# Kernel tuning notes

Measured on AMD Instinct MI355X. Metric: run time of the kernel, lower is better.

## Reference

```python
import jax, jax.numpy as jnp
import numpy as np
import math

D_MODEL, N_HEADS, D_HEAD = 768, 12, 64
INIT_RANGE = 0.02
ROPE_BASE = 10000.0


def _rope_cos_sin(seq_len, d_head, dtype=jnp.float32):
    # theta_j = base^(-2j/d), positions m -> angles [T, d/2]
    inv_freq = 1.0 / (ROPE_BASE ** (jnp.arange(0, d_head, 2, dtype=jnp.float32) / d_head))
    ang = jnp.arange(seq_len, dtype=jnp.float32)[:, None] * inv_freq[None, :]
    return jnp.cos(ang).astype(dtype), jnp.sin(ang).astype(dtype)


def _apply_rope(x, cos, sin):
    # x: [b, t, h, d]; rotate consecutive (even, odd) pairs as complex numbers
    xr, xi = x[..., 0::2], x[..., 1::2]
    c = cos[None, :, None, :]
    s = sin[None, :, None, :]
    out_r = xr * c - xi * s
    out_i = xr * s + xi * c
    return jnp.stack([out_r, out_i], axis=-1).reshape(x.shape)


def setup_inputs() -> dict:
    key = jax.random.key(0)
    ks = jax.random.split(key, 5)
    B, T = 2, 2048
    x = jax.random.normal(ks[0], (B, T, D_MODEL), dtype=jnp.float32)
    W_Q = INIT_RANGE * jax.random.normal(ks[1], (N_HEADS, D_MODEL, D_HEAD), dtype=jnp.float32)
    W_K = INIT_RANGE * jax.random.normal(ks[2], (N_HEADS, D_MODEL, D_HEAD), dtype=jnp.float32)
    W_V = INIT_RANGE * jax.random.normal(ks[3], (N_HEADS, D_MODEL, D_HEAD), dtype=jnp.float32)
    W_O = INIT_RANGE * jax.random.normal(ks[4], (N_HEADS, D_HEAD, D_MODEL), dtype=jnp.float32)
    b_Q = jnp.zeros((N_HEADS, D_HEAD), dtype=jnp.float32)
    b_K = jnp.zeros((N_HEADS, D_HEAD), dtype=jnp.float32)
    b_V = jnp.zeros((N_HEADS, D_HEAD), dtype=jnp.float32)
    b_O = jnp.zeros((D_MODEL,), dtype=jnp.float32)
    return {"normalized_resid_pre": x, "W_Q": W_Q, "b_Q": b_Q, "W_K": W_K, "b_K": b_K,
            "W_V": W_V, "b_V": b_V, "W_O": W_O, "b_O": b_O}


def reference(normalized_resid_pre, W_Q, b_Q, W_K, b_K, W_V, b_V, W_O, b_O):
    x = normalized_resid_pre
    B, T, _ = x.shape
    cos, sin = _rope_cos_sin(T, D_HEAD, x.dtype)
    Q = jnp.einsum('btc,hcd->bthd', x, W_Q) + b_Q
    K = jnp.einsum('btc,hcd->bthd', x, W_K) + b_K
    V = jnp.einsum('btc,hcd->bthd', x, W_V) + b_V
    Q = _apply_rope(Q, cos, sin)
    K = _apply_rope(K, cos, sin)
    scores = jnp.einsum('bqhd,bkhd->bhqk', Q, K) / math.sqrt(D_HEAD)
    # Faithful to source: tril zeros upper triangle, then all exact zeros -> -inf
    tril = jnp.tril(jnp.ones((T, T), dtype=bool))
    z = jnp.where(tril[None, None], scores, 0.0)
    z = jnp.where(z == 0.0, -jnp.inf, z)
    probs = jax.nn.softmax(z, axis=-1)
    o = jnp.einsum('bhqk,bkhd->bqhd', probs, V)
    return jnp.einsum('bqhd,hdm->bqm', o, W_O) + b_O
```

## Files before the change

### kernel.cpp

```cpp
#include <hip/hip_runtime.h>

typedef unsigned short u16;
typedef unsigned int u32;
typedef short bf16x8 __attribute__((ext_vector_type(8)));
typedef float f32x4 __attribute__((ext_vector_type(4)));
typedef float f32x16 __attribute__((ext_vector_type(16)));

#define MFMA(a, b, c) __builtin_amdgcn_mfma_f32_16x16x32_bf16(a, b, c, 0, 0, 0)
#define MFMA32(a, b, c) __builtin_amdgcn_mfma_f32_32x32x16_bf16(a, b, c, 0, 0, 0)

__device__ __forceinline__ u16 f2bf(float f) {
  unsigned int u = __float_as_uint(f);
  u = (u + 0x7FFFu + ((u >> 16) & 1u)) >> 16;
  return (u16)u;
}

#define GLOAD16(gp, lp)                                                        \
  __builtin_amdgcn_global_load_lds(                                            \
      (const __attribute__((address_space(1))) void*)(gp),                     \
      (__attribute__((address_space(3))) void*)(lp), 16, 0, 0)


__global__ void rope_tables(float* __restrict__ cost, float* __restrict__ sint) {
  int idx = blockIdx.x * 256 + threadIdx.x;
  if (idx >= 2048 * 32) return;
  int t = idx >> 5, i = idx & 31;
  float invf = expf(-(float)i * 0.28782313662425572f);
  float ang = (float)t * invf;
  cost[idx] = cosf(ang);
  sint[idx] = sinf(ang);
}

__global__ void cast_x(const float* __restrict__ x, u16* __restrict__ xb, int n) {
  int i = (blockIdx.x * 256 + threadIdx.x) * 4;
  if (i >= n) return;
  float4 v = *(const float4*)(x + i);
  u16 o0 = f2bf(v.x), o1 = f2bf(v.y), o2 = f2bf(v.z), o3 = f2bf(v.w);
  ushort4 o = make_ushort4(o0, o1, o2, o3);
  *(ushort4*)(xb + i) = o;
}

__global__ void prep_wqkv(const float* __restrict__ WQ, const float* __restrict__ WK,
                          const float* __restrict__ WV, u16* __restrict__ Wt) {
  __shared__ float tile[32][33];
  const int z = blockIdx.z;
  const int qkv = z / 12, h = z - qkv * 12;
  const float* W = (qkv == 0 ? WQ : qkv == 1 ? WK : WV) + (size_t)h * 768 * 64;
  const int k0 = blockIdx.x * 32, d0 = blockIdx.y * 32;
  const int tx = threadIdx.x, ty = threadIdx.y;
#pragma unroll
  for (int it = 0; it < 4; it++)
    tile[ty + it * 8][tx] = W[(size_t)(k0 + ty + it * 8) * 64 + d0 + tx];
  __syncthreads();
  u16* out = Wt + (size_t)(qkv * 768 + h * 64 + d0) * 768 + k0;
#pragma unroll
  for (int it = 0; it < 4; it++)
    out[(size_t)(ty + it * 8) * 768 + tx] = f2bf(tile[tx][ty + it * 8]);
}

__global__ void prep_wo(const float* __restrict__ WO, u16* __restrict__ Wt) {
  __shared__ float tile[32][33];
  const int a0 = blockIdx.x * 32, m0 = blockIdx.y * 32;
  const int tx = threadIdx.x, ty = threadIdx.y;
#pragma unroll
  for (int it = 0; it < 4; it++)
    tile[ty + it * 8][tx] = WO[(size_t)(a0 + ty + it * 8) * 768 + m0 + tx];
  __syncthreads();
#pragma unroll
  for (int it = 0; it < 4; it++)
    Wt[(size_t)(m0 + ty + it * 8) * 768 + a0 + tx] = f2bf(tile[tx][ty + it * 8]);
}

template <int MODE>
__global__ __launch_bounds__(256) void gemm_bt(
    const u16* __restrict__ A, const u16* __restrict__ Bt, int K, int LDA, int LDB,
    const float* __restrict__ bQ, const float* __restrict__ bK, const float* __restrict__ bV,
    const float* __restrict__ cost, const float* __restrict__ sint,
    u16* __restrict__ Qb, u16* __restrict__ Kb, u16* __restrict__ Vt,
    const float* __restrict__ bO, float* __restrict__ Out) {
  __shared__ u16 As[128 * 32];
  __shared__ u16 Bs[128 * 32];
  const int tid = threadIdx.x;
  const int w = tid >> 6, l = tid & 63;
  const int lr = l >> 4, lc = l & 15;
  const int wr = w >> 1, wc = w & 1;
  const int m0 = blockIdx.x * 128, n0 = blockIdx.y * 128;

  f32x4 acc[4][4];
#pragma unroll
  for (int mi = 0; mi < 4; mi++)
#pragma unroll
    for (int ni = 0; ni < 4; ni++) acc[mi][ni] = (f32x4){0.f, 0.f, 0.f, 0.f};

  for (int kt = 0; kt < K; kt += 32) {
    const u16* ga = A + (size_t)(m0 + w * 16 + (l >> 2)) * LDA + kt + (l & 3) * 8;
    const u16* gb = Bt + (size_t)(n0 + w * 16 + (l >> 2)) * LDB + kt + (l & 3) * 8;
    GLOAD16(ga, &As[w * 512]);
    GLOAD16(ga + (size_t)64 * LDA, &As[2048 + w * 512]);
    GLOAD16(gb, &Bs[w * 512]);
    GLOAD16(gb + (size_t)64 * LDB, &Bs[2048 + w * 512]);
    __syncthreads();

    bf16x8 af[4], bfr[4];
#pragma unroll
    for (int mi = 0; mi < 4; mi++)
      af[mi] = *(const bf16x8*)&As[(wr * 64 + mi * 16 + lc) * 32 + lr * 8];
#pragma unroll
    for (int ni = 0; ni < 4; ni++)
      bfr[ni] = *(const bf16x8*)&Bs[(wc * 64 + ni * 16 + lc) * 32 + lr * 8];
#pragma unroll
    for (int mi = 0; mi < 4; mi++)
#pragma unroll
      for (int ni = 0; ni < 4; ni++)
        acc[mi][ni] = MFMA(af[mi], bfr[ni], acc[mi][ni]);
    __syncthreads();
  }

#pragma unroll
  for (int mi = 0; mi < 4; mi++) {
#pragma unroll
    for (int ni = 0; ni < 4; ni++) {
      const int col = n0 + wc * 64 + ni * 16 + lc;
      const int rowb = m0 + wr * 64 + mi * 16 + lr * 4;
      if (MODE == 0) {
        const int qkv = col / 768;
        const int rem = col - qkv * 768;
        const int h = rem >> 6, d = rem & 63, fi = d >> 1;
        const float bb = (qkv == 0 ? bQ : qkv == 1 ? bK : bV)[rem];
#pragma unroll
        for (int r = 0; r < 4; r++) {
          const int grow = rowb + r;
          const int t = grow & 2047;
          float v = acc[mi][ni][r] + bb;
          float pv = __shfl_xor(v, 1);
          if (qkv < 2) {
            const float c = cost[t * 32 + fi], s = sint[t * 32 + fi];
            float o = (d & 1) ? (pv * s + v * c) : (v * c - pv * s);
            if (qkv == 0) o *= 0.125f;
            (qkv == 0 ? Qb : Kb)[(size_t)grow * 768 + rem] = f2bf(o);
          } else {
            const int bidx = grow >> 11;
            Vt[((size_t)(bidx * 12 + h) * 64 + d) * 2048 + t] = f2bf(v);
          }
        }
      } else {
        const float bb = bO[col];
#pragma unroll
        for (int r = 0; r < 4; r++) {
          const int grow = rowb + r;
          Out[(size_t)grow * 768 + col] = acc[mi][ni][r] + bb;
        }
      }
    }
  }
}

__global__ __launch_bounds__(256, 2) void attn_kernel(
    const u16* __restrict__ Qb, const u16* __restrict__ Kb,
    const u16* __restrict__ Vt, u16* __restrict__ Ob) {
  __shared__ char Kls[4][8192];
  __shared__ char Vls[4][8192];
  char* scratch = (char*)Kls;

  const int id = blockIdx.x + 16 * blockIdx.y;
  const int s_ = id >> 3;
  const int bh = (id & 7) + 8 * (s_ % 3);
  const int xq = s_ / 3;
  const int b = bh / 12, h = bh - b * 12;
  const int tid = threadIdx.x, w = tid >> 6, l = tid & 63;
  const int lq = l & 31, hi = l >> 5;
  const int qhalf = w & 1, grp = w >> 1;

  const u16* kbase = Kb + (size_t)(b * 2048) * 768 + h * 64;
  const u16* vbase = Vt + (size_t)(bh * 64) * 2048;

  const int r8 = l >> 3;
  const int scol8 = (l & 7) ^ r8;
  const u16* ksrc = kbase + (size_t)(w * 16 + r8) * 768 + scol8 * 8;
  const u16* vsrc = vbase + (size_t)(w * 16 + r8) * 2048 + scol8 * 8;

#define STAGE(t, bi)                                                        \
  {                                                                         \
    const size_t ko = (size_t)(t) * 64 * 768;                               \
    const int vo = (t) * 64;                                                \
    GLOAD16(ksrc + ko,            &Kls[bi][w * 2048]);                      \
    GLOAD16(ksrc + ko + 8 * 768,  &Kls[bi][w * 2048 + 1024]);               \
    GLOAD16(vsrc + vo,            &Vls[bi][w * 2048]);                      \
    GLOAD16(vsrc + vo + 8 * 2048, &Vls[bi][w * 2048 + 1024]);               \
  }

  const int fswz = (lq & 7) << 4;

#pragma unroll 1
  for (int half = 0; half < 2; half++) {
    const int qblk = half == 0 ? 31 - xq : xq;
    const int n = qblk + 1;
    const int nsup = (n + 1) >> 1;

    bf16x8 qf[4];
    {
      const u16* qp = Qb + ((size_t)(b * 2048 + qblk * 64 + qhalf * 32 + lq)) * 768 +
                      h * 64 + hi * 8;
#pragma unroll
      for (int c = 0; c < 4; c++) qf[c] = *(const bf16x8*)(qp + c * 16);
    }

    float m_run = -INFINITY, l_run = 0.f;
    f32x16 acc2[2];
    acc2[0] = (f32x16)0.0f;
    acc2[1] = (f32x16)0.0f;

    STAGE(0, 0);
    if (n > 1) STAGE(1, 1);

    for (int p = 0; p < nsup; p++) {
      const int t0 = 2 * p;
      asm volatile("s_waitcnt vmcnt(0)" ::: "memory");
      __builtin_amdgcn_s_barrier();
      __builtin_amdgcn_sched_barrier(0);
      if (t0 + 2 < n) STAGE(t0 + 2, (t0 + 2) & 3);
      if (t0 + 3 < n) STAGE(t0 + 3, (t0 + 3) & 3);

      const int tile = t0 + grp;
      if (tile < n) {
        const int cur = tile & 3;

        f32x16 s2[2];
        s2[0] = (f32x16)0.0f;
        s2[1] = (f32x16)0.0f;
        __builtin_amdgcn_s_setprio(1);
#pragma unroll
        for (int c = 0; c < 4; c++) {
          const int cb = (c * 32 + hi * 16) ^ fswz;
          bf16x8 kf0 = *(const bf16x8*)(&Kls[cur][lq * 128] + cb);
          bf16x8 kf1 = *(const bf16x8*)(&Kls[cur][(32 + lq) * 128] + cb);
          s2[0] = MFMA32(kf0, qf[c], s2[0]);
          s2[1] = MFMA32(kf1, qf[c], s2[1]);
        }
        __builtin_amdgcn_s_setprio(0);

        if (tile == qblk) {
          const int qrel = qhalf * 32 + lq;
#pragma unroll
          for (int kt2 = 0; kt2 < 2; kt2++)
#pragma unroll
            for (int r = 0; r < 16; r++) {
              const int ko = kt2 * 32 + (r & 3) + 8 * (r >> 2) + 4 * hi;
              if (ko > qrel) s2[kt2][r] = -INFINITY;
            }
        }

        float pm = s2[0][0];
#pragma unroll
        for (int r = 1; r < 16; r++) pm = fmaxf(pm, s2[0][r]);
#pragma unroll
        for (int r = 0; r < 16; r++) pm = fmaxf(pm, s2[1][r]);
        pm = fmaxf(pm, __shfl_xor(pm, 32));

        const float mn = fmaxf(m_run, pm);
        const float alpha = __expf(m_run - mn);
        m_run = mn;

        float rs = 0.f;
        u32 pk[2][8];
#pragma unroll
        for (int kt2 = 0; kt2 < 2; kt2++)
#pragma unroll
          for (int j = 0; j < 8; j++) {
            float p0 = __expf(s2[kt2][2 * j] - mn);
            float p1 = __expf(s2[kt2][2 * j + 1] - mn);
            rs += p0 + p1;
            asm("v_cvt_pk_bf16_f32 %0, %1, %2" : "=v"(pk[kt2][j]) : "v"(p0), "v"(p1));
          }
        l_run = l_run * alpha + rs;

        union { u32 u[4]; bf16x8 v; } pf[4];
#pragma unroll
        for (int kq = 0; kq < 4; kq++) {
          const int kt2 = kq >> 1, i0 = 4 * (kq & 1);
          u32 a0 = pk[kt2][i0], b0 = pk[kt2][i0 + 2];
          u32 a1 = pk[kt2][i0 + 1], b1 = pk[kt2][i0 + 3];
          asm("v_permlane32_swap_b32 %0, %1" : "+v"(a0), "+v"(b0));
          asm("v_permlane32_swap_b32 %0, %1" : "+v"(a1), "+v"(b1));
          pf[kq].u[0] = a0; pf[kq].u[1] = a1; pf[kq].u[2] = b0; pf[kq].u[3] = b1;
        }

#pragma unroll
        for (int dh = 0; dh < 2; dh++)
#pragma unroll
          for (int r = 0; r < 16; r++) acc2[dh][r] *= alpha;

        __builtin_amdgcn_s_setprio(1);
#pragma unroll
        for (int dh = 0; dh < 2; dh++) {
          const char* vr = &Vls[cur][(dh * 32 + lq) * 128];
#pragma unroll
          for (int kq = 0; kq < 4; kq++) {
            bf16x8 vf = *(const bf16x8*)(vr + ((kq * 32 + hi * 16) ^ fswz));
            acc2[dh] = MFMA32(vf, pf[kq].v, acc2[dh]);
          }
        }
        __builtin_amdgcn_s_setprio(0);
      }
    }

    asm volatile("s_waitcnt lgkmcnt(0)" ::: "memory");
    __builtin_amdgcn_s_barrier();
    if (grp == 1) {
      float* sc = (float*)scratch + ((size_t)(w - 2) * 64 + l) * 34;
#pragma unroll
      for (int dh = 0; dh < 2; dh++)
#pragma unroll
        for (int r = 0; r < 16; r++) sc[dh * 16 + r] = acc2[dh][r];
      sc[32] = m_run;
      sc[33] = l_run;
    }
    asm volatile("s_waitcnt lgkmcnt(0)" ::: "memory");
    __builtin_amdgcn_s_barrier();
    if (grp == 0) {
      const float* sc = (const float*)scratch + ((size_t)w * 64 + l) * 34;
      const float m1 = sc[32], l1 = sc[33];
      const float M = fmaxf(m_run, m1);
      const float a0 = __expf(m_run - M);
      const float a1 = __expf(m1 - M);
      const float lm = l_run * a0 + l1 * a1;
      const float lt = lm + __shfl_xor(lm, 32);
      const float inv = 1.0f / lt;
      u16* ob = Ob + ((size_t)(b * 2048 + qblk * 64 + qhalf * 32 + lq)) * 768 + h * 64;
#pragma unroll
      for (int dh = 0; dh < 2; dh++)
#pragma unroll
        for (int g = 0; g < 4; g++) {
          ushort4 o4;
          o4.x = f2bf((acc2[dh][4 * g + 0] * a0 + sc[dh * 16 + 4 * g + 0] * a1) * inv);
          o4.y = f2bf((acc2[dh][4 * g + 1] * a0 + sc[dh * 16 + 4 * g + 1] * a1) * inv);
          o4.z = f2bf((acc2[dh][4 * g + 2] * a0 + sc[dh * 16 + 4 * g + 2] * a1) * inv);
          o4.w = f2bf((acc2[dh][4 * g + 3] * a0 + sc[dh * 16 + 4 * g + 3] * a1) * inv);
          *(ushort4*)(ob + dh * 32 + 8 * g + 4 * hi) = o4;
        }
    }
    asm volatile("s_waitcnt lgkmcnt(0)" ::: "memory");
    __builtin_amdgcn_s_barrier();
  }
#undef STAGE
}


extern "C" void kernel_launch(void* const* d_in, const int* in_sizes, int n_in,
                              void* d_out, int out_size, void* d_ws, size_t ws_size,
                              hipStream_t stream) {
  const float* x  = (const float*)d_in[0];
  const float* WQ = (const float*)d_in[1];
  const float* bQ = (const float*)d_in[2];
  const float* WK = (const float*)d_in[3];
  const float* bK = (const float*)d_in[4];
  const float* WV = (const float*)d_in[5];
  const float* bV = (const float*)d_in[6];
  const float* WO = (const float*)d_in[7];
  const float* bO = (const float*)d_in[8];

  char* ws = (char*)d_ws;
  u16* Xb    = (u16*)(ws + 0);
  u16* Wqkv  = (u16*)(ws + 6291456);
  u16* WoT   = (u16*)(ws + 9830400);
  u16* Qb    = (u16*)(ws + 11010048);
  u16* Kb    = (u16*)(ws + 17301504);
  u16* Vt    = (u16*)(ws + 23592960);
  u16* Ob    = (u16*)(ws + 29884416);
  float* cost = (float*)(ws + 36175872);
  float* sint = (float*)(ws + 36438016);

  rope_tables<<<256, 256, 0, stream>>>(cost, sint);
  cast_x<<<3072, 256, 0, stream>>>(x, Xb, 4096 * 768);
  prep_wqkv<<<dim3(24, 2, 36), dim3(32, 8), 0, stream>>>(WQ, WK, WV, Wqkv);
  prep_wo<<<dim3(24, 24), dim3(32, 8), 0, stream>>>(WO, WoT);

  gemm_bt<0><<<dim3(32, 18), 256, 0, stream>>>(Xb, Wqkv, 768, 768, 768,
                                               bQ, bK, bV, cost, sint,
                                               Qb, Kb, Vt, nullptr, nullptr);
  attn_kernel<<<dim3(16, 24), 256, 0, stream>>>(Qb, Kb, Vt, Ob);
  gemm_bt<1><<<dim3(32, 6), 256, 0, stream>>>(Ob, WoT, 768, 768, 768,
                                              nullptr, nullptr, nullptr, nullptr, nullptr,
                                              nullptr, nullptr, nullptr, bO, (float*)d_out);
}
```

Baseline: 119.1 us.

## Triple-buffer GEMM LDS tiles with swizzle and XCD-aware block remap

Result: faster. 115.8 us (-2.8%).

```diff
diff --git a/kernel.cpp b/kernel.cpp
--- a/kernel.cpp
+++ b/kernel.cpp
@@ -78,13 +78,17 @@
     const float* __restrict__ cost, const float* __restrict__ sint,
     u16* __restrict__ Qb, u16* __restrict__ Kb, u16* __restrict__ Vt,
     const float* __restrict__ bO, float* __restrict__ Out) {
-  __shared__ u16 As[128 * 32];
-  __shared__ u16 Bs[128 * 32];
+  __shared__ u16 As[3][128 * 32];
+  __shared__ u16 Bs[3][128 * 32];
   const int tid = threadIdx.x;
   const int w = tid >> 6, l = tid & 63;
   const int lr = l >> 4, lc = l & 15;
   const int wr = w >> 1, wc = w & 1;
-  const int m0 = blockIdx.x * 128, n0 = blockIdx.y * 128;
+
+  const int id = blockIdx.x + (int)gridDim.x * blockIdx.y;
+  const int xcd = id & 7, idx = id >> 3;
+  const int m0 = (xcd * 4 + (idx & 3)) * 128;
+  const int n0 = (idx >> 2) * 128;
 
   f32x4 acc[4][4];
 #pragma unroll
@@ -92,29 +96,53 @@
 #pragma unroll
     for (int ni = 0; ni < 4; ni++) acc[mi][ni] = (f32x4){0.f, 0.f, 0.f, 0.f};
 
-  for (int kt = 0; kt < K; kt += 32) {
-    const u16* ga = A + (size_t)(m0 + w * 16 + (l >> 2)) * LDA + kt + (l & 3) * 8;
-    const u16* gb = Bt + (size_t)(n0 + w * 16 + (l >> 2)) * LDB + kt + (l & 3) * 8;
-    GLOAD16(ga, &As[w * 512]);
-    GLOAD16(ga + (size_t)64 * LDA, &As[2048 + w * 512]);
-    GLOAD16(gb, &Bs[w * 512]);
-    GLOAD16(gb + (size_t)64 * LDB, &Bs[2048 + w * 512]);
-    __syncthreads();
-
+  const int srow = w * 16 + (l >> 2);
+  const int sg = (l & 3) ^ ((l >> 3) & 3);
+  const u16* ga = A + (size_t)(m0 + srow) * LDA + sg * 8;
+  const u16* gb = Bt + (size_t)(n0 + srow) * LDB + sg * 8;
+
+#define GSTAGE(t, bi)                                                   \
+  {                                                                     \
+    const int kk = (t) * 32;                                            \
+    GLOAD16(ga + kk, &As[bi][w * 512]);                                 \
+    GLOAD16(ga + kk + (size_t)64 * LDA, &As[bi][2048 + w * 512]);       \
+    GLOAD16(gb + kk, &Bs[bi][w * 512]);                                 \
+    GLOAD16(gb + kk + (size_t)64 * LDB, &Bs[bi][2048 + w * 512]);       \
+  }
+
+  const int n = K >> 5;
+  GSTAGE(0, 0);
+  if (n > 1) GSTAGE(1, 1);
+
+  for (int kt = 0; kt < n; kt++) {
+    if (kt + 1 < n) asm volatile("s_waitcnt vmcnt(4)" ::: "memory");
+    else            asm volatile("s_waitcnt vmcnt(0)" ::: "memory");
+    __builtin_amdgcn_s_barrier();
+    __builtin_amdgcn_sched_barrier(0);
+    if (kt + 2 < n) GSTAGE(kt + 2, (kt + 2) % 3);
+
+    const char* as = (const char*)As[kt % 3];
+    const char* bs = (const char*)Bs[kt % 3];
     bf16x8 af[4], bfr[4];
 #pragma unroll
-    for (int mi = 0; mi < 4; mi++)
-      af[mi] = *(const bf16x8*)&As[(wr * 64 + mi * 16 + lc) * 32 + lr * 8];
-#pragma unroll
-    for (int ni = 0; ni < 4; ni++)
-      bfr[ni] = *(const bf16x8*)&Bs[(wc * 64 + ni * 16 + lc) * 32 + lr * 8];
+    for (int mi = 0; mi < 4; mi++) {
+      const int row = wr * 64 + mi * 16 + lc;
+      af[mi] = *(const bf16x8*)(as + row * 64 + ((lr ^ ((row >> 1) & 3)) << 4));
+    }
+#pragma unroll
+    for (int ni = 0; ni < 4; ni++) {
+      const int row = wc * 64 + ni * 16 + lc;
+      bfr[ni] = *(const bf16x8*)(bs + row * 64 + ((lr ^ ((row >> 1) & 3)) << 4));
+    }
+    __builtin_amdgcn_s_setprio(1);
 #pragma unroll
     for (int mi = 0; mi < 4; mi++)
 #pragma unroll
       for (int ni = 0; ni < 4; ni++)
         acc[mi][ni] = MFMA(af[mi], bfr[ni], acc[mi][ni]);
-    __syncthreads();
+    __builtin_amdgcn_s_setprio(0);
   }
+#undef GSTAGE
 
 #pragma unroll
   for (int mi = 0; mi < 4; mi++) {
```
